# Performance work log

Measured on AMD Instinct MI355X. Metric: run time of the kernel, lower is better.

## Reference

```python
import jax, jax.numpy as jnp
import numpy as np

B, S, D = 2, 2048, 1024
H, DH = 16, 64  # num_heads, hidden_dimension (per-head)


def setup_inputs() -> dict:
    key = jax.random.key(0)
    ks = jax.random.split(key, 9)
    s = 1.0 / np.sqrt(D)
    so = 1.0 / np.sqrt(H * DH)
    return {
        "x": jax.random.normal(ks[0], (B, S, D), dtype=jnp.float32),
        "Wq": jax.random.uniform(ks[1], (D, H * DH), jnp.float32, -s, s),
        "bq": jax.random.uniform(ks[2], (H * DH,), jnp.float32, -s, s),
        "Wk": jax.random.uniform(ks[3], (D, H * DH), jnp.float32, -s, s),
        "bk": jax.random.uniform(ks[4], (H * DH,), jnp.float32, -s, s),
        "Wv": jax.random.uniform(ks[5], (D, H * DH), jnp.float32, -s, s),
        "bv": jax.random.uniform(ks[6], (H * DH,), jnp.float32, -s, s),
        "Wo": jax.random.uniform(ks[7], (H * DH, D), jnp.float32, -so, so),
        "bo": jax.random.uniform(ks[8], (D,), jnp.float32, -so, so),
    }


def reference(x, Wq, bq, Wk, bk, Wv, bv, Wo, bo):
    b, s, _ = x.shape
    # project and split heads: [b, h, s, dh]
    q = (x @ Wq + bq).reshape(b, s, H, DH).transpose(0, 2, 1, 3)
    k = (x @ Wk + bk).reshape(b, s, H, DH).transpose(0, 2, 1, 3)
    v = (x @ Wv + bv).reshape(b, s, H, DH).transpose(0, 2, 1, 3)
    scores = jnp.einsum('bhqd,bhkd->bhqk', q, k) / jnp.sqrt(jnp.float32(DH))
    causal = jnp.triu(jnp.ones((s, s), dtype=bool), k=1)
    scores = jnp.where(causal, -jnp.inf, scores)
    weights = jax.nn.softmax(scores, axis=-1)
    out = jnp.einsum('bhqk,bhkd->bhqd', weights, v)
    out = out.transpose(0, 2, 1, 3).reshape(b, s, H * DH)
    return out @ Wo + bo
```

## Files before the change

### kernel.cpp

```cpp
#include <hip/hip_runtime.h>

#define B_  2
#define S_  2048
#define D_  1024
#define H_  16
#define DH_ 64
#define NDH (H_*DH_)
#define BS_ (B_*S_)
#define PER ((size_t)B_*H_*S_*DH_)

typedef __bf16 bf16;
typedef bf16 bf16x8 __attribute__((ext_vector_type(8)));
typedef bf16 bf16x4 __attribute__((ext_vector_type(4)));
typedef float f32x4 __attribute__((ext_vector_type(4)));

#define AS1 __attribute__((address_space(1)))
#define AS3 __attribute__((address_space(3)))
__device__ inline void gld16(const bf16* g, bf16* l) {
    __builtin_amdgcn_global_load_lds((const AS1 void*)g, (AS3 void*)l, 16, 0, 0);
}

__global__ void cast_bf16(const float* __restrict__ in, bf16* __restrict__ out, int n) {
    int i = (blockIdx.x * blockDim.x + threadIdx.x) * 4;
    if (i < n) {
        float4 v = *(const float4*)(in + i);
        bf16x4 o = { (bf16)v.x, (bf16)v.y, (bf16)v.z, (bf16)v.w };
        *(bf16x4*)(out + i) = o;
    }
}

__global__ void transW4(const float* __restrict__ W0, const float* __restrict__ W1,
                        const float* __restrict__ W2, const float* __restrict__ W3,
                        bf16* __restrict__ T0, bf16* __restrict__ T1,
                        bf16* __restrict__ T2, bf16* __restrict__ T3) {
    int z = blockIdx.z;
    const float* W = (z == 0) ? W0 : (z == 1) ? W1 : (z == 2) ? W2 : W3;
    bf16* Wt = (z == 0) ? T0 : (z == 1) ? T1 : (z == 2) ? T2 : T3;
    __shared__ float T[32][33];
    int k0 = blockIdx.y * 32, n0 = blockIdx.x * 32;
    int t = threadIdx.x;
    int r = t >> 3, c = (t & 7) * 4;
    float4 v = *(const float4*)(W + (size_t)(k0 + r) * 1024 + n0 + c);
    T[c + 0][r] = v.x; T[c + 1][r] = v.y; T[c + 2][r] = v.z; T[c + 3][r] = v.w;
    __syncthreads();
    bf16x4 o = { (bf16)T[r][c], (bf16)T[r][c + 1], (bf16)T[r][c + 2], (bf16)T[r][c + 3] };
    *(bf16x4*)(Wt + (size_t)(n0 + r) * 1024 + k0 + c) = o;
}

__global__ __launch_bounds__(256) void qkv_gemm(
        const bf16* __restrict__ A, const bf16* __restrict__ Bt,
        const float* __restrict__ bq, const float* __restrict__ bk,
        const float* __restrict__ bv, bf16* __restrict__ Qout, bf16* __restrict__ Vt) {
    __shared__ __align__(16) bf16 As[128 * 32];
    __shared__ __align__(16) bf16 Bs[128 * 32];
    int tid = threadIdx.x, wave = tid >> 6, lane = tid & 63;
    int quad = lane >> 4, l16 = lane & 15;
    int bm = blockIdx.y * 128, bn = blockIdx.x * 128;
    int wm = (wave >> 1) * 64, wn = (wave & 1) * 64;

    int sr = lane >> 2, sc = (lane & 3) * 8;
    const bf16* Ag0 = A + (size_t)(bm + (wave * 2 + 0) * 16 + sr) * 1024 + sc;
    const bf16* Ag1 = A + (size_t)(bm + (wave * 2 + 1) * 16 + sr) * 1024 + sc;
    const bf16* Bg0 = Bt + (size_t)(bn + (wave * 2 + 0) * 16 + sr) * 1024 + sc;
    const bf16* Bg1 = Bt + (size_t)(bn + (wave * 2 + 1) * 16 + sr) * 1024 + sc;
    bf16* Al0 = &As[(wave * 2 + 0) * 512];
    bf16* Al1 = &As[(wave * 2 + 1) * 512];
    bf16* Bl0 = &Bs[(wave * 2 + 0) * 512];
    bf16* Bl1 = &Bs[(wave * 2 + 1) * 512];

    f32x4 acc[4][4] = {};

    for (int k0 = 0; k0 < 1024; k0 += 32) {
        gld16(Ag0 + k0, Al0);
        gld16(Ag1 + k0, Al1);
        gld16(Bg0 + k0, Bl0);
        gld16(Bg1 + k0, Bl1);
        __syncthreads();
        bf16x8 af[4], bfr[4];
        #pragma unroll
        for (int i = 0; i < 4; ++i)
            af[i] = *(const bf16x8*)&As[(wm + i * 16 + l16) * 32 + quad * 8];
        #pragma unroll
        for (int j = 0; j < 4; ++j)
            bfr[j] = *(const bf16x8*)&Bs[(wn + j * 16 + l16) * 32 + quad * 8];
        #pragma unroll
        for (int i = 0; i < 4; ++i)
          #pragma unroll
          for (int j = 0; j < 4; ++j)
            acc[i][j] = __builtin_amdgcn_mfma_f32_16x16x32_bf16(af[i], bfr[j], acc[i][j], 0, 0, 0);
        __syncthreads();
    }

    #pragma unroll
    for (int i = 0; i < 4; ++i)
      #pragma unroll
      for (int j = 0; j < 4; ++j) {
        int col = bn + wn + j * 16 + l16;
        float bias = (col < 1024) ? bq[col] : (col < 2048) ? bk[col - 1024] : bv[col - 2048];
        int qkv = col >> 10, cw = col & 1023;
        int hh = cw >> 6, d = cw & 63;
        int row0 = bm + wm + i * 16 + quad * 4;
        int bb = row0 >> 11, s0 = row0 & 2047;
        if (qkv < 2) {
            #pragma unroll
            for (int r = 0; r < 4; ++r)
                Qout[(size_t)qkv * PER + (((size_t)bb * H_ + hh) * S_ + s0 + r) * DH_ + d] =
                    (bf16)(acc[i][j][r] + bias);
        } else {
            bf16x4 pack;
            #pragma unroll
            for (int r = 0; r < 4; ++r) pack[r] = (bf16)(acc[i][j][r] + bias);
            *(bf16x4*)&Vt[(((size_t)bb * H_ + hh) * DH_ + d) * S_ + s0] = pack;
        }
      }
}

__global__ __launch_bounds__(256) void gemm128f(
        const bf16* __restrict__ A, const bf16* __restrict__ Bt,
        const float* __restrict__ bias, float* __restrict__ out) {
    __shared__ __align__(16) bf16 As[128 * 32];
    __shared__ __align__(16) bf16 Bs[128 * 32];
    int tid = threadIdx.x, wave = tid >> 6, lane = tid & 63;
    int quad = lane >> 4, l16 = lane & 15;
    int bm = blockIdx.y * 128, bn = blockIdx.x * 128;
    int wm = (wave >> 1) * 64, wn = (wave & 1) * 64;

    int sr = lane >> 2, sc = (lane & 3) * 8;
    const bf16* Ag0 = A + (size_t)(bm + (wave * 2 + 0) * 16 + sr) * 1024 + sc;
    const bf16* Ag1 = A + (size_t)(bm + (wave * 2 + 1) * 16 + sr) * 1024 + sc;
    const bf16* Bg0 = Bt + (size_t)(bn + (wave * 2 + 0) * 16 + sr) * 1024 + sc;
    const bf16* Bg1 = Bt + (size_t)(bn + (wave * 2 + 1) * 16 + sr) * 1024 + sc;
    bf16* Al0 = &As[(wave * 2 + 0) * 512];
    bf16* Al1 = &As[(wave * 2 + 1) * 512];
    bf16* Bl0 = &Bs[(wave * 2 + 0) * 512];
    bf16* Bl1 = &Bs[(wave * 2 + 1) * 512];

    f32x4 acc[4][4] = {};

    for (int k0 = 0; k0 < 1024; k0 += 32) {
        gld16(Ag0 + k0, Al0);
        gld16(Ag1 + k0, Al1);
        gld16(Bg0 + k0, Bl0);
        gld16(Bg1 + k0, Bl1);
        __syncthreads();
        bf16x8 af[4], bfr[4];
        #pragma unroll
        for (int i = 0; i < 4; ++i)
            af[i] = *(const bf16x8*)&As[(wm + i * 16 + l16) * 32 + quad * 8];
        #pragma unroll
        for (int j = 0; j < 4; ++j)
            bfr[j] = *(const bf16x8*)&Bs[(wn + j * 16 + l16) * 32 + quad * 8];
        #pragma unroll
        for (int i = 0; i < 4; ++i)
          #pragma unroll
          for (int j = 0; j < 4; ++j)
            acc[i][j] = __builtin_amdgcn_mfma_f32_16x16x32_bf16(af[i], bfr[j], acc[i][j], 0, 0, 0);
        __syncthreads();
    }

    #pragma unroll
    for (int i = 0; i < 4; ++i)
      #pragma unroll
      for (int j = 0; j < 4; ++j) {
        int col = bn + wn + j * 16 + l16;
        float b = bias[col];
        #pragma unroll
        for (int r = 0; r < 4; ++r) {
            int row = bm + wm + i * 16 + quad * 4 + r;
            out[(size_t)row * 1024 + col] = acc[i][j][r] + b;
        }
      }
}

__global__ __launch_bounds__(256) void flash3(
        const bf16* __restrict__ Q, const bf16* __restrict__ K,
        const bf16* __restrict__ Vt, bf16* __restrict__ O) {
    int bh = blockIdx.x;
    int b = bh >> 4, h = bh & 15;
    int tile = 63 - (int)blockIdx.y;
    int q0 = tile * 32;
    int tid = threadIdx.x;
    int wave = tid >> 6, lane = tid & 63;
    int quad = lane >> 4, l16 = lane & 15;

    __shared__ __align__(16) char smem[4 * 2 * 16 * 72 * 2];
    bf16 (*P)[2][16][72] = reinterpret_cast<bf16 (*)[2][16][72]>(smem);
    float (*redO)[4][64][4] = reinterpret_cast<float (*)[4][64][4]>(smem);
    __shared__ float redL[4][2][4][4];

    const bf16* Qb = Q + (size_t)bh * S_ * DH_;
    const bf16* Kb = K + (size_t)bh * S_ * DH_;
    const bf16* Vb = Vt + (size_t)bh * DH_ * S_;

    bf16x8 qf[2][2];
    #pragma unroll
    for (int s = 0; s < 2; ++s) {
        const bf16* qp = Qb + (size_t)(q0 + s * 16 + l16) * DH_ + quad * 8;
        qf[s][0] = *(const bf16x8*)(qp);
        qf[s][1] = *(const bf16x8*)(qp + 32);
    }

    bf16x8 ones;
    #pragma unroll
    for (int j = 0; j < 8; ++j) ones[j] = (l16 == 0) ? (bf16)1.0f : (bf16)0.0f;

    f32x4 oacc[2][4] = {};
    f32x4 lacc[2] = {};

    int nkt = tile / 2 + 1;
    for (int kt = wave; kt < nkt; kt += 4) {
        int kv0 = kt * 64;
        bf16x8 kf[4][2];
        #pragma unroll
        for (int ns = 0; ns < 4; ++ns) {
            const bf16* kp = Kb + (size_t)(kv0 + ns * 16 + l16) * DH_ + quad * 8;
            kf[ns][0] = *(const bf16x8*)(kp);
            kf[ns][1] = *(const bf16x8*)(kp + 32);
        }
        f32x4 sacc[2][4] = {};
        #pragma unroll
        for (int s = 0; s < 2; ++s)
          #pragma unroll
          for (int ns = 0; ns < 4; ++ns) {
            sacc[s][ns] = __builtin_amdgcn_mfma_f32_16x16x32_bf16(qf[s][0], kf[ns][0], sacc[s][ns], 0, 0, 0);
            sacc[s][ns] = __builtin_amdgcn_mfma_f32_16x16x32_bf16(qf[s][1], kf[ns][1], sacc[s][ns], 0, 0, 0);
          }
        bool diag = (kt == nkt - 1);
        #pragma unroll
        for (int s = 0; s < 2; ++s)
          #pragma unroll
          for (int ns = 0; ns < 4; ++ns)
            #pragma unroll
            for (int r = 0; r < 4; ++r) {
                float p = __expf(sacc[s][ns][r] * 0.125f);
                if (diag) {
                    int kv = kv0 + ns * 16 + l16;
                    int qq = q0 + s * 16 + quad * 4 + r;
                    if (kv > qq) p = 0.f;
                }
                P[wave][s][quad * 4 + r][ns * 16 + l16] = (bf16)p;
            }
        #pragma unroll
        for (int ks = 0; ks < 2; ++ks) {
            bf16x8 pf0 = *(const bf16x8*)&P[wave][0][l16][ks * 32 + quad * 8];
            bf16x8 pf1 = *(const bf16x8*)&P[wave][1][l16][ks * 32 + quad * 8];
            lacc[0] = __builtin_amdgcn_mfma_f32_16x16x32_bf16(pf0, ones, lacc[0], 0, 0, 0);
            lacc[1] = __builtin_amdgcn_mfma_f32_16x16x32_bf16(pf1, ones, lacc[1], 0, 0, 0);
            #pragma unroll
            for (int ds = 0; ds < 4; ++ds) {
                bf16x8 vf = *(const bf16x8*)(Vb + (size_t)(ds * 16 + l16) * S_ + kv0 + ks * 32 + quad * 8);
                oacc[0][ds] = __builtin_amdgcn_mfma_f32_16x16x32_bf16(pf0, vf, oacc[0][ds], 0, 0, 0);
                oacc[1][ds] = __builtin_amdgcn_mfma_f32_16x16x32_bf16(pf1, vf, oacc[1][ds], 0, 0, 0);
            }
        }
    }

    if (l16 == 0) {
        #pragma unroll
        for (int s = 0; s < 2; ++s)
          #pragma unroll
          for (int r = 0; r < 4; ++r)
            redL[wave][s][quad][r] = lacc[s][r];
    }
    #pragma unroll
    for (int s = 0; s < 2; ++s) {
        __syncthreads();
        #pragma unroll
        for (int ds = 0; ds < 4; ++ds)
            *(f32x4*)&redO[wave][ds][lane][0] = oacc[s][ds];
        __syncthreads();
        f32x4 osum = {};
        #pragma unroll
        for (int w = 0; w < 4; ++w)
            osum += *(const f32x4*)&redO[w][wave][lane][0];
        #pragma unroll
        for (int r = 0; r < 4; ++r) {
            float lsum = redL[0][s][quad][r] + redL[1][s][quad][r]
                       + redL[2][s][quad][r] + redL[3][s][quad][r];
            int qq = q0 + s * 16 + quad * 4 + r;
            O[((size_t)b * S_ + qq) * NDH + h * DH_ + wave * 16 + l16] = (bf16)(osum[r] / lsum);
        }
    }
}

extern "C" void kernel_launch(void* const* d_in, const int* in_sizes, int n_in,
                              void* d_out, int out_size, void* d_ws, size_t ws_size,
                              hipStream_t stream) {
    const float* x  = (const float*)d_in[0];
    const float* Wq = (const float*)d_in[1];
    const float* bq = (const float*)d_in[2];
    const float* Wk = (const float*)d_in[3];
    const float* bk = (const float*)d_in[4];
    const float* Wv = (const float*)d_in[5];
    const float* bv = (const float*)d_in[6];
    const float* Wo = (const float*)d_in[7];
    const float* bo = (const float*)d_in[8];
    float* out = (float*)d_out;

    bf16* ws = (bf16*)d_ws;
    const size_t M1 = (size_t)1024 * 1024;
    bf16* xb    = ws;
    bf16* WqkvT = ws + 4 * M1;
    bf16* WoT   = ws + 7 * M1;
    bf16* Qw    = ws + 8 * M1;
    bf16* Vtw   = ws + 16 * M1;
    bf16* Ow    = ws + 20 * M1;

    int nx = BS_ * D_;
    cast_bf16<<<nx / 4 / 256, 256, 0, stream>>>(x, xb, nx);
    transW4<<<dim3(32, 32, 4), 256, 0, stream>>>(Wq, Wk, Wv, Wo,
                                                 WqkvT, WqkvT + M1, WqkvT + 2 * M1, WoT);

    qkv_gemm<<<dim3(3072 / 128, BS_ / 128), 256, 0, stream>>>(xb, WqkvT, bq, bk, bv, Qw, Vtw);

    flash3<<<dim3(B_ * H_, 64), 256, 0, stream>>>(Qw, Qw + PER, Vtw, Ow);

    gemm128f<<<dim3(1024 / 128, BS_ / 128), 256, 0, stream>>>(Ow, WoT, bo, out);
}
```

Measured before the change: 224.2 us.

## Fuse prep kernels and pair causal tiles per attention block

The x cast and weight transpose kernels are merged into one launch, with the block index choosing which job a block does. This removes one kernel launch and its gap. The attention kernel now has each block process two query tiles, tile pr and tile 63-pr, so every block does the same total causal work, and the grid is halved. This evens out load across blocks but removes half the parallelism, and the tiles inside a block run one after the other, joined by a barrier.

```diff
diff --git a/kernel.cpp b/kernel.cpp
--- a/kernel.cpp
+++ b/kernel.cpp
@@ -20,25 +20,26 @@
     __builtin_amdgcn_global_load_lds((const AS1 void*)g, (AS3 void*)l, 16, 0, 0);
 }
 
-__global__ void cast_bf16(const float* __restrict__ in, bf16* __restrict__ out, int n) {
-    int i = (blockIdx.x * blockDim.x + threadIdx.x) * 4;
-    if (i < n) {
-        float4 v = *(const float4*)(in + i);
+__global__ __launch_bounds__(256) void prep(
+        const float* __restrict__ x,
+        const float* __restrict__ W0, const float* __restrict__ W1,
+        const float* __restrict__ W2, const float* __restrict__ W3,
+        bf16* __restrict__ xb, bf16* __restrict__ T0, bf16* __restrict__ T1,
+        bf16* __restrict__ T2, bf16* __restrict__ T3) {
+    __shared__ float T[32][33];
+    int bid = blockIdx.x, t = threadIdx.x;
+    if (bid < 4096) {
+        int i = (bid * 256 + t) * 4;
+        float4 v = *(const float4*)(x + i);
         bf16x4 o = { (bf16)v.x, (bf16)v.y, (bf16)v.z, (bf16)v.w };
-        *(bf16x4*)(out + i) = o;
+        *(bf16x4*)(xb + i) = o;
+        return;
     }
-}
-
-__global__ void transW4(const float* __restrict__ W0, const float* __restrict__ W1,
-                        const float* __restrict__ W2, const float* __restrict__ W3,
-                        bf16* __restrict__ T0, bf16* __restrict__ T1,
-                        bf16* __restrict__ T2, bf16* __restrict__ T3) {
-    int z = blockIdx.z;
+    int r2 = bid - 4096;
+    int z = r2 >> 10, w = r2 & 1023;
     const float* W = (z == 0) ? W0 : (z == 1) ? W1 : (z == 2) ? W2 : W3;
     bf16* Wt = (z == 0) ? T0 : (z == 1) ? T1 : (z == 2) ? T2 : T3;
-    __shared__ float T[32][33];
-    int k0 = blockIdx.y * 32, n0 = blockIdx.x * 32;
-    int t = threadIdx.x;
+    int k0 = (w >> 5) * 32, n0 = (w & 31) * 32;
     int r = t >> 3, c = (t & 7) * 4;
     float4 v = *(const float4*)(W + (size_t)(k0 + r) * 1024 + n0 + c);
     T[c + 0][r] = v.x; T[c + 1][r] = v.y; T[c + 2][r] = v.z; T[c + 3][r] = v.w;
@@ -172,13 +173,12 @@
       }
 }
 
-__global__ __launch_bounds__(256) void flash3(
+__global__ __launch_bounds__(256) void flash4(
         const bf16* __restrict__ Q, const bf16* __restrict__ K,
         const bf16* __restrict__ Vt, bf16* __restrict__ O) {
     int bh = blockIdx.x;
     int b = bh >> 4, h = bh & 15;
-    int tile = 63 - (int)blockIdx.y;
-    int q0 = tile * 32;
+    int pr = blockIdx.y;
     int tid = threadIdx.x;
     int wave = tid >> 6, lane = tid & 63;
     int quad = lane >> 4, l16 = lane & 15;
@@ -192,94 +192,100 @@
     const bf16* Kb = K + (size_t)bh * S_ * DH_;
     const bf16* Vb = Vt + (size_t)bh * DH_ * S_;
 
-    bf16x8 qf[2][2];
-    #pragma unroll
-    for (int s = 0; s < 2; ++s) {
-        const bf16* qp = Qb + (size_t)(q0 + s * 16 + l16) * DH_ + quad * 8;
-        qf[s][0] = *(const bf16x8*)(qp);
-        qf[s][1] = *(const bf16x8*)(qp + 32);
-    }
-
     bf16x8 ones;
     #pragma unroll
     for (int j = 0; j < 8; ++j) ones[j] = (l16 == 0) ? (bf16)1.0f : (bf16)0.0f;
 
-    f32x4 oacc[2][4] = {};
-    f32x4 lacc[2] = {};
-
-    int nkt = tile / 2 + 1;
-    for (int kt = wave; kt < nkt; kt += 4) {
-        int kv0 = kt * 64;
-        bf16x8 kf[4][2];
-        #pragma unroll
-        for (int ns = 0; ns < 4; ++ns) {
-            const bf16* kp = Kb + (size_t)(kv0 + ns * 16 + l16) * DH_ + quad * 8;
-            kf[ns][0] = *(const bf16x8*)(kp);
-            kf[ns][1] = *(const bf16x8*)(kp + 32);
-        }
-        f32x4 sacc[2][4] = {};
-        #pragma unroll
-        for (int s = 0; s < 2; ++s)
-          #pragma unroll
-          for (int ns = 0; ns < 4; ++ns) {
-            sacc[s][ns] = __builtin_amdgcn_mfma_f32_16x16x32_bf16(qf[s][0], kf[ns][0], sacc[s][ns], 0, 0, 0);
-            sacc[s][ns] = __builtin_amdgcn_mfma_f32_16x16x32_bf16(qf[s][1], kf[ns][1], sacc[s][ns], 0, 0, 0);
-          }
-        bool diag = (kt == nkt - 1);
-        #pragma unroll
-        for (int s = 0; s < 2; ++s)
-          #pragma unroll
-          for (int ns = 0; ns < 4; ++ns)
+    for (int half = 0; half < 2; ++half) {
+        int tile = half ? (63 - pr) : pr;
+        int q0 = tile * 32;
+
+        bf16x8 qf[2][2];
+        #pragma unroll
+        for (int s = 0; s < 2; ++s) {
+            const bf16* qp = Qb + (size_t)(q0 + s * 16 + l16) * DH_ + quad * 8;
+            qf[s][0] = *(const bf16x8*)(qp);
+            qf[s][1] = *(const bf16x8*)(qp + 32);
+        }
+
+        f32x4 oacc[2][4] = {};
+        f32x4 lacc[2] = {};
+
+        int nkt = tile / 2 + 1;
+        for (int kt = wave; kt < nkt; kt += 4) {
+            int kv0 = kt * 64;
+            bf16x8 kf[4][2];
+            #pragma unroll
+            for (int ns = 0; ns < 4; ++ns) {
+                const bf16* kp = Kb + (size_t)(kv0 + ns * 16 + l16) * DH_ + quad * 8;
+                kf[ns][0] = *(const bf16x8*)(kp);
+                kf[ns][1] = *(const bf16x8*)(kp + 32);
+            }
+            f32x4 sacc[2][4] = {};
+            #pragma unroll
+            for (int s = 0; s < 2; ++s)
+              #pragma unroll
+              for (int ns = 0; ns < 4; ++ns) {
+                sacc[s][ns] = __builtin_amdgcn_mfma_f32_16x16x32_bf16(qf[s][0], kf[ns][0], sacc[s][ns], 0, 0, 0);
+                sacc[s][ns] = __builtin_amdgcn_mfma_f32_16x16x32_bf16(qf[s][1], kf[ns][1], sacc[s][ns], 0, 0, 0);
+              }
+            bool diag = (kt == nkt - 1);
+            #pragma unroll
+            for (int s = 0; s < 2; ++s)
+              #pragma unroll
+              for (int ns = 0; ns < 4; ++ns)
+                #pragma unroll
+                for (int r = 0; r < 4; ++r) {
+                    float p = __expf(sacc[s][ns][r] * 0.125f);
+                    if (diag) {
+                        int kv = kv0 + ns * 16 + l16;
+                        int qq = q0 + s * 16 + quad * 4 + r;
+                        if (kv > qq) p = 0.f;
+                    }
+                    P[wave][s][quad * 4 + r][ns * 16 + l16] = (bf16)p;
+                }
+            #pragma unroll
+            for (int ks = 0; ks < 2; ++ks) {
+                bf16x8 pf0 = *(const bf16x8*)&P[wave][0][l16][ks * 32 + quad * 8];
+                bf16x8 pf1 = *(const bf16x8*)&P[wave][1][l16][ks * 32 + quad * 8];
+                lacc[0] = __builtin_amdgcn_mfma_f32_16x16x32_bf16(pf0, ones, lacc[0], 0, 0, 0);
+                lacc[1] = __builtin_amdgcn_mfma_f32_16x16x32_bf16(pf1, ones, lacc[1], 0, 0, 0);
+                #pragma unroll
+                for (int ds = 0; ds < 4; ++ds) {
+                    bf16x8 vf = *(const bf16x8*)(Vb + (size_t)(ds * 16 + l16) * S_ + kv0 + ks * 32 + quad * 8);
+                    oacc[0][ds] = __builtin_amdgcn_mfma_f32_16x16x32_bf16(pf0, vf, oacc[0][ds], 0, 0, 0);
+                    oacc[1][ds] = __builtin_amdgcn_mfma_f32_16x16x32_bf16(pf1, vf, oacc[1][ds], 0, 0, 0);
+                }
+            }
+        }
+
+        if (l16 == 0) {
+            #pragma unroll
+            for (int s = 0; s < 2; ++s)
+              #pragma unroll
+              for (int r = 0; r < 4; ++r)
+                redL[wave][s][quad][r] = lacc[s][r];
+        }
+        #pragma unroll
+        for (int s = 0; s < 2; ++s) {
+            __syncthreads();
+            #pragma unroll
+            for (int ds = 0; ds < 4; ++ds)
+                *(f32x4*)&redO[wave][ds][lane][0] = oacc[s][ds];
+            __syncthreads();
+            f32x4 osum = {};
+            #pragma unroll
+            for (int w = 0; w < 4; ++w)
+                osum += *(const f32x4*)&redO[w][wave][lane][0];
             #pragma unroll
             for (int r = 0; r < 4; ++r) {
-                float p = __expf(sacc[s][ns][r] * 0.125f);
-                if (diag) {
-                    int kv = kv0 + ns * 16 + l16;
-                    int qq = q0 + s * 16 + quad * 4 + r;
-                    if (kv > qq) p = 0.f;
-                }
-                P[wave][s][quad * 4 + r][ns * 16 + l16] = (bf16)p;
+                float lsum = redL[0][s][quad][r] + redL[1][s][quad][r]
+                           + redL[2][s][quad][r] + redL[3][s][quad][r];
+                int qq = q0 + s * 16 + quad * 4 + r;
+                O[((size_t)b * S_ + qq) * NDH + h * DH_ + wave * 16 + l16] = (bf16)(osum[r] / lsum);
             }
-        #pragma unroll
-        for (int ks = 0; ks < 2; ++ks) {
-            bf16x8 pf0 = *(const bf16x8*)&P[wave][0][l16][ks * 32 + quad * 8];
-            bf16x8 pf1 = *(const bf16x8*)&P[wave][1][l16][ks * 32 + quad * 8];
-            lacc[0] = __builtin_amdgcn_mfma_f32_16x16x32_bf16(pf0, ones, lacc[0], 0, 0, 0);
-            lacc[1] = __builtin_amdgcn_mfma_f32_16x16x32_bf16(pf1, ones, lacc[1], 0, 0, 0);
-            #pragma unroll
-            for (int ds = 0; ds < 4; ++ds) {
-                bf16x8 vf = *(const bf16x8*)(Vb + (size_t)(ds * 16 + l16) * S_ + kv0 + ks * 32 + quad * 8);
-                oacc[0][ds] = __builtin_amdgcn_mfma_f32_16x16x32_bf16(pf0, vf, oacc[0][ds], 0, 0, 0);
-                oacc[1][ds] = __builtin_amdgcn_mfma_f32_16x16x32_bf16(pf1, vf, oacc[1][ds], 0, 0, 0);
-            }
-        }
-    }
-
-    if (l16 == 0) {
-        #pragma unroll
-        for (int s = 0; s < 2; ++s)
-          #pragma unroll
-          for (int r = 0; r < 4; ++r)
-            redL[wave][s][quad][r] = lacc[s][r];
-    }
-    #pragma unroll
-    for (int s = 0; s < 2; ++s) {
-        __syncthreads();
-        #pragma unroll
-        for (int ds = 0; ds < 4; ++ds)
-            *(f32x4*)&redO[wave][ds][lane][0] = oacc[s][ds];
-        __syncthreads();
-        f32x4 osum = {};
-        #pragma unroll
-        for (int w = 0; w < 4; ++w)
-            osum += *(const f32x4*)&redO[w][wave][lane][0];
-        #pragma unroll
-        for (int r = 0; r < 4; ++r) {
-            float lsum = redL[0][s][quad][r] + redL[1][s][quad][r]
-                       + redL[2][s][quad][r] + redL[3][s][quad][r];
-            int qq = q0 + s * 16 + quad * 4 + r;
-            O[((size_t)b * S_ + qq) * NDH + h * DH_ + wave * 16 + l16] = (bf16)(osum[r] / lsum);
-        }
+        }
+        __syncthreads();
     }
 }
 
@@ -306,14 +312,12 @@
     bf16* Vtw   = ws + 16 * M1;
     bf16* Ow    = ws + 20 * M1;
 
-    int nx = BS_ * D_;
-    cast_bf16<<<nx / 4 / 256, 256, 0, stream>>>(x, xb, nx);
-    transW4<<<dim3(32, 32, 4), 256, 0, stream>>>(Wq, Wk, Wv, Wo,
-                                                 WqkvT, WqkvT + M1, WqkvT + 2 * M1, WoT);
+    prep<<<8192, 256, 0, stream>>>(x, Wq, Wk, Wv, Wo,
+                                   xb, WqkvT, WqkvT + M1, WqkvT + 2 * M1, WoT);
 
     qkv_gemm<<<dim3(3072 / 128, BS_ / 128), 256, 0, stream>>>(xb, WqkvT, bq, bk, bv, Qw, Vtw);
 
-    flash3<<<dim3(B_ * H_, 64), 256, 0, stream>>>(Qw, Qw + PER, Vtw, Ow);
+    flash4<<<dim3(B_ * H_, 32), 256, 0, stream>>>(Qw, Qw + PER, Vtw, Ow);
 
     gemm128f<<<dim3(1024 / 128, BS_ / 128), 256, 0, stream>>>(Ow, WoT, bo, out);
 }
```

Measured after the change: 219.5 us. -2.1%, faster.
